# Performance work log

Hardware: AMD Instinct MI355X
Metric: run time of the kernel (lower is better)

Reference implementation:

```python
import jax, jax.numpy as jnp
import numpy as np

C_P = 1004.0
R_EARTH = 6371000.0
R_GAS = 287.0
OMEGA_E = 7.292e-05
B, K, H, W = 1, 8, 361, 720
KK = 5   # kernel basis size
D = 5    # neighborhood width in lat and lon (radius 2)
NS = K * 4 + 1
FCH = K * 4
NU = 2.0e5  # diffusion coefficient


def _ch(k, kind):
    return k * 4 + kind


def disco_gather(x, psi, quad):
    # DISCO sparse neighborhood aggregation on the sphere.
    # x: (B,C,H,W); psi: (KK,2,H,D,D) lat-dependent filter basis (2 directional comps)
    # returns (B,C,KK,2,H,W)
    Bx, C, Hx, Wx = x.shape
    Kk, nc, _, Dlat, Dlon = psi.shape
    r = Dlat // 2
    lat = np.clip(np.arange(Hx)[:, None] + np.arange(Dlat)[None, :] - r, 0, Hx - 1)
    out = jnp.zeros((Bx, C, Kk, nc, Hx, Wx), x.dtype)
    for dl in range(Dlat):
        li = lat[:, dl]
        xg = x[:, :, li, :] * quad[li][None, None, :, None]  # quadrature-weighted gather
        for dw in range(Dlon):
            xs = jnp.roll(xg, -(dw - r), axis=-1)  # circular in longitude
            out = out + psi[:, :, :, dl, dw][None, None, :, :, :, None] * xs[:, :, None, None, :, :]
    return out


def setup_inputs():
    key = jax.random.key(0)
    k1, k2, k3 = jax.random.split(key, 3)
    uv = jax.random.normal(k1, (B, K, H, W, 2), jnp.float32)
    T = jax.random.normal(k2, (B, K, H, W), jnp.float32)
    q = jax.random.normal(k3, (B, K, H, W), jnp.float32)
    rng = np.random.RandomState(0)
    psi = ((rng.rand(KK, 2, H, D, D) - 0.5) / (D * D)).astype(np.float32)
    colat = np.linspace(0.0, np.pi, H)
    quad = (np.sin(colat) * np.pi / (H - 1)).astype(np.float32)
    f_cor = (2.0 * OMEGA_E * np.sin(np.pi / 2.0 - colat)).astype(np.float32)
    p = np.array([1e5 * np.exp(-k * np.log(10.0) / (K - 1)) for k in range(K)], np.float32)
    lpr = np.log(p[:-1] / p[1:])
    p_low = np.concatenate([p[:1], 0.5 * (p[:-1] + p[1:])])
    p_up = np.concatenate([0.5 * (p[:-1] + p[1:]), [0.0]])
    dp = (p_low - p_up).astype(np.float32)
    # physics-encoded weights (module freezes all params and sets them analytically)
    W_ss_blk = np.zeros((NS, NS, KK), np.float32)
    W_vs_blk = np.zeros((NS, K, KK, 2), np.float32)
    for k in range(K):
        W_vs_blk[_ch(k, 2), k, :, 0] = 1.0 / R_EARTH  # zeta (curl)
        W_vs_blk[_ch(k, 3), k, :, 1] = 1.0 / R_EARTH  # div
    W_sv_blk = np.zeros((K, NS, KK, 2), np.float32)
    for ko in range(K):
        for ki in range(ko):
            W_sv_blk[ko, _ch(ki, 0), :, 1] = -R_GAS * lpr[ki] / R_EARTH  # PGF
        W_sv_blk[ko, _ch(ko, 1), :, 1] = -1.0 / R_EARTH  # -grad KE
    W_vv_blk = np.zeros((K, K, KK, 2), np.float32)
    W_vs2_blk = np.zeros((NS, K, KK, 2), np.float32)
    W_pw_ss = np.zeros((NS, NS), np.float32)
    W_pw_ss[FCH, FCH] = 1.0
    W_svp = np.zeros((NS, K, 2), np.float32)
    for k in range(K):
        W_svp[_ch(k, 2), k, 1] = 1.0
    W_svp[FCH, :, 1] = -1.0
    W_pw_vv = np.zeros((K, K), np.float32)
    W_ss_adv = np.zeros((2 * K, 2 * K, KK), np.float32)
    W_vs_adv = np.zeros((2 * K, K, KK, 2), np.float32)
    W_vs2_adv = np.zeros((2 * K, K, KK, 2), np.float32)
    for k in range(K):
        W_vs2_adv[k, k, :, 1] = -1.0 / R_EARTH      # -V.grad T
        W_vs2_adv[K + k, k, :, 1] = -1.0 / R_EARTH  # -V.grad q
    W_sv_grad = np.zeros((1, 1, KK, 2), np.float32)
    W_sv_grad[0, 0, :, 1] = 1.0 / R_EARTH
    W_vs_div = np.zeros((1, 1, KK, 2), np.float32)
    W_vs_div[0, 0, :, 1] = 1.0 / R_EARTH
    j = jnp.asarray
    return dict(uv=uv, T=T, q=q, psi=j(psi), quad=j(quad), f_cor=j(f_cor), p_levels=j(p), delta_p=j(dp),
                W_ss_blk=j(W_ss_blk), W_vs_blk=j(W_vs_blk), W_sv_blk=j(W_sv_blk), W_vv_blk=j(W_vv_blk),
                W_vs2_blk=j(W_vs2_blk), W_pw_ss=j(W_pw_ss), W_svp=j(W_svp), W_pw_vv=j(W_pw_vv),
                W_ss_adv=j(W_ss_adv), W_vs_adv=j(W_vs_adv), W_vs2_adv=j(W_vs2_adv),
                W_sv_grad=j(W_sv_grad), W_vs_div=j(W_vs_div))


def _forward(uv, T, q, psi, quad, f_cor, p_levels, delta_p, W_ss_blk, W_vs_blk, W_sv_blk, W_vv_blk,
             W_vs2_blk, W_pw_ss, W_svp, W_pw_vv, W_ss_adv, W_vs_adv, W_vs2_adv, W_sv_grad, W_vs_div):
    Bx, Kx, Hx, Wx = T.shape
    ke = 0.5 * (uv[..., 0] ** 2 + uv[..., 1] ** 2)
    zeros = jnp.zeros_like(T)
    per = jnp.stack([T, ke, zeros, zeros], axis=2).reshape(Bx, Kx * 4, Hx, Wx)
    f_field = jnp.broadcast_to(f_cor[None, None, :, None], (Bx, 1, Hx, Wx))
    x_s = jnp.concatenate([per, f_field], axis=1)  # (B, 4K+1, H, W)
    # ---- Block 1: VectorDiscoBlock ----
    Gs = disco_gather(x_s, psi, quad)               # (B,NS,KK,2,H,W)
    Ga = disco_gather(uv[..., 0], psi, quad)
    Gb = disco_gather(uv[..., 1], psi, quad)
    Gdir = jnp.stack([Ga[:, :, :, 0], Gb[:, :, :, 1]], axis=3)  # curl/div pairing
    Giso = jnp.stack([Ga[:, :, :, 0], Gb[:, :, :, 0]], axis=3)
    ys_c = jnp.einsum('oik,bikhw->bohw', W_ss_blk, Gs[:, :, :, 0])
    ys_c = ys_c + jnp.einsum('oikc,bikchw->bohw', W_vs_blk, Gdir)
    ys_c = ys_c + jnp.einsum('oikc,bokchw,bihwc->bohw', W_vs2_blk, Gs, uv)
    yv_c = jnp.einsum('oikc,bikchw->bohwc', W_sv_blk, Gs)
    yv_c = yv_c + jnp.einsum('oikc,bikchw->bohwc', W_vv_blk, Giso)
    s_feat = ys_c + jnp.einsum('oi,bihw->bohw', W_pw_ss, x_s)
    coef0 = jnp.einsum('ij,bihw->bjhw', W_svp[:, :, 0], s_feat)
    coef1 = jnp.einsum('ij,bihw->bjhw', W_svp[:, :, 1], s_feat)
    cross = jnp.stack([-uv[..., 1], uv[..., 0]], axis=-1)  # k-hat x V
    sv = coef0[..., None] * uv + coef1[..., None] * cross
    y_v = uv + yv_c + sv + jnp.einsum('oi,bihwc->bohwc', W_pw_vv, uv)
    y_s = s_feat
    duv_dt = y_v - uv
    # omega from divergence (upward pressure integral)
    div = y_s[:, :Kx * 4].reshape(Bx, Kx, 4, Hx, Wx)[:, :, 3]
    cum = jnp.cumsum(div * delta_p[None, :, None, None], axis=1)
    omega = 0.5 * (jnp.concatenate([jnp.zeros_like(cum[:, :1]), cum[:, :-1]], axis=1) + cum)
    # ---- adv_conv (W_vs2 pathway): -V.grad(T), -V.grad(q) ----
    tq = jnp.concatenate([T, q], axis=1)
    Gtq = disco_gather(tq, psi, quad)
    dTq = jnp.einsum('oik,bikhw->bohw', W_ss_adv, Gtq[:, :, :, 0])
    dTq = dTq + jnp.einsum('oikc,bikchw->bohw', W_vs_adv, Gdir)
    dTq = dTq + jnp.einsum('oikc,bokchw,bihwc->bohw', W_vs2_adv, Gtq, uv)
    dT_dt = dTq[:, :Kx]
    dq_dt = dTq[:, Kx:]
    # dT/dp central differences
    p = p_levels
    inter = (T[:, 2:] - T[:, :-2]) / (p[2:] - p[:-2])[None, :, None, None]
    first = (T[:, 1:2] - T[:, 0:1]) / (p[1] - p[0])
    last = (T[:, -1:] - T[:, -2:-1]) / (p[-1] - p[-2])
    dTdp = jnp.concatenate([first, inter, last], axis=1)
    pk = p[None, :, None, None]
    dT_dt = dT_dt + omega * (R_GAS / C_P * T / pk - dTdp)
    # ---- diffusion: nu * div(grad(s)) via grad_conv/div_conv ----
    def lap(s):
        sf = s.reshape(Bx * Kx, 1, Hx, Wx)
        Gsf = disco_gather(sf, psi, quad)
        g = jnp.einsum('oikc,bikchw->bohwc', W_sv_grad, Gsf)  # (BK,1,H,W,2)
        Gga = disco_gather(g[..., 0], psi, quad)
        Ggb = disco_gather(g[..., 1], psi, quad)
        Gd = jnp.stack([Gga[:, :, :, 0], Ggb[:, :, :, 1]], axis=3)
        return jnp.einsum('oikc,bikchw->bohw', W_vs_div, Gd).reshape(Bx, Kx, Hx, Wx)
    dT_dt = dT_dt + NU * lap(T)
    dq_dt = dq_dt + NU * lap(q)
    duv_dt = duv_dt + NU * jnp.stack([lap(uv[..., 0]), lap(uv[..., 1])], axis=-1)
    return duv_dt, dT_dt, dq_dt


def reference(uv, T, q, psi, quad, f_cor, p_levels, delta_p, W_ss_blk, W_vs_blk, W_sv_blk, W_vv_blk,
              W_vs2_blk, W_pw_ss, W_svp, W_pw_vv, W_ss_adv, W_vs_adv, W_vs2_adv, W_sv_grad, W_vs_div):
    return _forward(uv, T, q, psi, quad, f_cor, p_levels, delta_p, W_ss_blk, W_vs_blk, W_sv_blk,
                    W_vv_blk, W_vs2_blk, W_pw_ss, W_svp, W_pw_vv, W_ss_adv, W_vs_adv, W_vs2_adv,
                    W_sv_grad, W_vs_div)
```

## Files before the change

kernel.cpp:

```cpp
#include <hip/hip_runtime.h>


constexpr int Kz = 8, Hh = 361, Ww = 720;
constexpr int HW = Hh * Ww;
constexpr int OFF_DT = Kz * HW * 2;
constexpr int OFF_DQ = OFF_DT + Kz * HW;

constexpr int TH = 32, TW = 32;
constexpr int NTHR = 256;
constexpr int NCOL = 8;
constexpr int SH = TH + 8, SW4 = TW + 8;
constexpr int EH = TH + 4, EW4 = TW + 4;
constexpr int SW4P = 41;
constexpr int EW4P = 37;
constexpr int PQROW = 40;
constexpr int GX = (Ww + TW - 1) / TW;
constexpr int GY = (Hh + TH - 1) / TH;

__device__ __forceinline__ int clipH(int x) {
  return x < 0 ? 0 : (x > Hh - 1 ? Hh - 1 : x);
}

#define FMA4(acc, s, v)                                                        \
  do {                                                                         \
    acc.x = fmaf((s), (v).x, acc.x);                                           \
    acc.y = fmaf((s), (v).y, acc.y);                                           \
    acc.z = fmaf((s), (v).z, acc.z);                                           \
    acc.w = fmaf((s), (v).w, acc.w);                                           \
  } while (0)

#define ROWV(acc, a, b, c, d, e)                                               \
  do {                                                                         \
    FMA4(acc, wq0, a); FMA4(acc, wq1, b); FMA4(acc, wq2, c);                   \
    FMA4(acc, wq3, d); FMA4(acc, wq4, e);                                      \
  } while (0)

#define ROW5S(acc, q0, q1, q2, q3, q4, a, b, c, d, e)                          \
  acc = fmaf(q0, a, fmaf(q1, b, fmaf(q2, c, fmaf(q3, d, fmaf(q4, e, acc)))))

__global__ __launch_bounds__(256) void pe_tab_pq(
    const float* __restrict__ psi,
    const float* __restrict__ quad,
    float* __restrict__ P0g,
    float* __restrict__ P1g)
{
  int idx = blockIdx.x * 256 + threadIdx.x;
  if (idx >= Hh * PQROW) return;
  int h = idx / PQROW, o = idx - h * PQROW;
  int a = o >> 3, b = o & 7;
  float v0 = 0.f, v1 = 0.f;
  if (b < 5) {
    #pragma unroll
    for (int kk = 0; kk < 5; ++kk) {
      v0 += psi[kk * (2 * Hh * 25) + h * 25 + a * 5 + b];
      v1 += psi[kk * (2 * Hh * 25) + Hh * 25 + h * 25 + a * 5 + b];
    }
    float qv = quad[clipH(h + a - 2)];
    v0 *= qv; v1 *= qv;
  }
  P0g[idx] = v0;
  P1g[idx] = v1;
}

__global__ __launch_bounds__(NTHR) void pe_pass1(
    const float2* __restrict__ uv,
    const float*  __restrict__ Tg,
    const float*  __restrict__ qg,
    const float*  __restrict__ P0g,
    const float*  __restrict__ P1g,
    const float*  __restrict__ f_cor,
    const float*  __restrict__ delta_p,
    float* __restrict__ out,
    float2* __restrict__ ws)
{
  __shared__ float4 S4[SH][SW4P];
  __shared__ float4 d1S[EH][EW4P];

  const int tid = threadIdx.x;
  const int tx = tid % NCOL;
  const int ty = tid / NCOL;
  const int w0 = blockIdx.x * TW;
  const int h0 = blockIdx.y * TH;
  const int k  = blockIdx.z;

  for (int idx = tid; idx < SH * SW4; idx += NTHR) {
    int rr = idx / SW4, cc = idx - rr * SW4;
    int pr = clipH(h0 + rr - 4);
    int pc = w0 + cc - 4;
    pc = pc < 0 ? pc + Ww : (pc >= Ww ? pc - Ww : pc);
    int g = (k * Hh + pr) * Ww + pc;
    float2 uvv = uv[g];
    S4[rr][cc] = make_float4(uvv.x, uvv.y, Tg[g], qg[g]);
  }
  __syncthreads();

  for (int idx = tid; idx < EH * (EW4 / 4); idx += NTHR) {
    int ee = idx % EH;
    int gc = idx / EH;
    int cb = gc * 4;
    int p = clipH(h0 + ee - 2);
    const float* Pr = P1g + p * PQROW;
    float4 a0 = {0,0,0,0}, a1 = {0,0,0,0}, a2 = {0,0,0,0}, a3 = {0,0,0,0};
    #pragma unroll
    for (int dl = 0; dl < 5; ++dl) {
      int sp = clipH(p + dl - 2);
      int rr = sp - h0 + 4;
      const float4* row = &S4[rr][cb];
      float4 g0 = row[0], g1 = row[1], g2 = row[2], g3 = row[3];
      float4 g4 = row[4], g5 = row[5], g6 = row[6], g7 = row[7];
      float4 wA = *(const float4*)(Pr + dl * 8);
      float wq0 = wA.x, wq1 = wA.y, wq2 = wA.z, wq3 = wA.w;
      float wq4 = Pr[dl * 8 + 4];
      ROWV(a0, g0, g1, g2, g3, g4);
      ROWV(a1, g1, g2, g3, g4, g5);
      ROWV(a2, g2, g3, g4, g5, g6);
      ROWV(a3, g3, g4, g5, g6, g7);
    }
    d1S[ee][cb + 0] = a0; d1S[ee][cb + 1] = a1;
    d1S[ee][cb + 2] = a2; d1S[ee][cb + 3] = a3;
  }
  __syncthreads();

  const int h = h0 + ty;
  const int hc = h < Hh ? h : (Hh - 1);
  const int wbase = w0 + tx * 4;
  const float f = f_cor[hc];
  const float invR = (float)(1.0 / 6371000.0);
  const float halfInvR = 0.5f * invR;
  const float cL = 200000.0f * invR * invR;
  const float* Pr1 = P1g + hc * PQROW;
  const float* Pr0 = P0g + hc * PQROW;

  float4 lp0 = {0,0,0,0}, lp1 = {0,0,0,0}, lp2 = {0,0,0,0}, lp3 = {0,0,0,0};
  float du0 = 0.f, du1 = 0.f, du2 = 0.f, du3 = 0.f;
  float dk0 = 0.f, dk1 = 0.f, dk2 = 0.f, dk3 = 0.f;
  #pragma unroll
  for (int dl = 0; dl < 5; ++dl) {
    int sp = clipH(hc + dl - 2);
    int er = sp - h0 + 2;
    int rr = er + 2;
    float4 wA = *(const float4*)(Pr1 + dl * 8);
    float wq0 = wA.x, wq1 = wA.y, wq2 = wA.z, wq3 = wA.w;
    float wq4 = Pr1[dl * 8 + 4];
    {
      const float4* row = &d1S[er][tx * 4];
      float4 g0 = row[0], g1 = row[1], g2 = row[2], g3 = row[3];
      float4 g4 = row[4], g5 = row[5], g6 = row[6], g7 = row[7];
      ROWV(lp0, g0, g1, g2, g3, g4);
      ROWV(lp1, g1, g2, g3, g4, g5);
      ROWV(lp2, g2, g3, g4, g5, g6);
      ROWV(lp3, g3, g4, g5, g6, g7);
    }
    {
      const float4* srow = &S4[rr][tx * 4 + 2];
      float4 s0 = srow[0], s1 = srow[1], s2 = srow[2], s3 = srow[3];
      float4 s4 = srow[4], s5 = srow[5], s6 = srow[6], s7 = srow[7];
      float k0 = fmaf(s0.y, s0.y, s0.x * s0.x);
      float k1 = fmaf(s1.y, s1.y, s1.x * s1.x);
      float k2 = fmaf(s2.y, s2.y, s2.x * s2.x);
      float k3 = fmaf(s3.y, s3.y, s3.x * s3.x);
      float k4 = fmaf(s4.y, s4.y, s4.x * s4.x);
      float k5 = fmaf(s5.y, s5.y, s5.x * s5.x);
      float k6 = fmaf(s6.y, s6.y, s6.x * s6.x);
      float k7 = fmaf(s7.y, s7.y, s7.x * s7.x);
      ROW5S(dk0, wq0, wq1, wq2, wq3, wq4, k0, k1, k2, k3, k4);
      ROW5S(dk1, wq0, wq1, wq2, wq3, wq4, k1, k2, k3, k4, k5);
      ROW5S(dk2, wq0, wq1, wq2, wq3, wq4, k2, k3, k4, k5, k6);
      ROW5S(dk3, wq0, wq1, wq2, wq3, wq4, k3, k4, k5, k6, k7);
      float4 w0A = *(const float4*)(Pr0 + dl * 8);
      float q0 = w0A.x, q1 = w0A.y, q2 = w0A.z, q3 = w0A.w;
      float q4 = Pr0[dl * 8 + 4];
      ROW5S(du0, q0, q1, q2, q3, q4, s0.x, s1.x, s2.x, s3.x, s4.x);
      ROW5S(du1, q0, q1, q2, q3, q4, s1.x, s2.x, s3.x, s4.x, s5.x);
      ROW5S(du2, q0, q1, q2, q3, q4, s2.x, s3.x, s4.x, s5.x, s6.x);
      ROW5S(du3, q0, q1, q2, q3, q4, s3.x, s4.x, s5.x, s6.x, s7.x);
    }
  }

  if (h < Hh && wbase < Ww) {
    const float dpk = delta_p[k];
    float4 duvA, duvB, dTv, dqv, wsA, wsB;
    {
      float4 d1c = d1S[ty + 2][tx * 4 + 2];
      float4 ctr = S4[ty + 4][tx * 4 + 4];
      float coef1 = fmaf(du0, invR, -f);
      duvA.x = fmaf(-coef1, ctr.y, cL * lp0.x);
      duvA.y = fmaf(coef1, ctr.x, -halfInvR * dk0) + cL * lp0.y;
      dTv.x = -(invR * d1c.z) * ctr.y + cL * lp0.z;
      dqv.x = fmaf(-(invR * d1c.w), ctr.y, cL * lp0.w);
      wsA.x = invR * d1c.y * dpk; wsA.y = d1c.z;
    }
    {
      float4 d1c = d1S[ty + 2][tx * 4 + 3];
      float4 ctr = S4[ty + 4][tx * 4 + 5];
      float coef1 = fmaf(du1, invR, -f);
      duvA.z = fmaf(-coef1, ctr.y, cL * lp1.x);
      duvA.w = fmaf(coef1, ctr.x, -halfInvR * dk1) + cL * lp1.y;
      dTv.y = -(invR * d1c.z) * ctr.y + cL * lp1.z;
      dqv.y = fmaf(-(invR * d1c.w), ctr.y, cL * lp1.w);
      wsA.z = invR * d1c.y * dpk; wsA.w = d1c.z;
    }
    {
      float4 d1c = d1S[ty + 2][tx * 4 + 4];
      float4 ctr = S4[ty + 4][tx * 4 + 6];
      float coef1 = fmaf(du2, invR, -f);
      duvB.x = fmaf(-coef1, ctr.y, cL * lp2.x);
      duvB.y = fmaf(coef1, ctr.x, -halfInvR * dk2) + cL * lp2.y;
      dTv.z = -(invR * d1c.z) * ctr.y + cL * lp2.z;
      dqv.z = fmaf(-(invR * d1c.w), ctr.y, cL * lp2.w);
      wsB.x = invR * d1c.y * dpk; wsB.y = d1c.z;
    }
    {
      float4 d1c = d1S[ty + 2][tx * 4 + 5];
      float4 ctr = S4[ty + 4][tx * 4 + 7];
      float coef1 = fmaf(du3, invR, -f);
      duvB.z = fmaf(-coef1, ctr.y, cL * lp3.x);
      duvB.w = fmaf(coef1, ctr.x, -halfInvR * dk3) + cL * lp3.y;
      dTv.w = -(invR * d1c.z) * ctr.y + cL * lp3.z;
      dqv.w = fmaf(-(invR * d1c.w), ctr.y, cL * lp3.w);
      wsB.z = invR * d1c.y * dpk; wsB.w = d1c.z;
    }
    const int gidx = (k * Hh + h) * Ww + wbase;
    float4* o4 = (float4*)out;
    o4[gidx >> 1] = duvA;
    o4[(gidx >> 1) + 1] = duvB;
    *(float4*)&out[OFF_DT + gidx] = dTv;
    *(float4*)&out[OFF_DQ + gidx] = dqv;
    float4* w4 = (float4*)ws;
    w4[gidx >> 1] = wsA;
    w4[(gidx >> 1) + 1] = wsB;
  }
}

__global__ __launch_bounds__(256) void pe_pass2(
    const float* __restrict__ Tg,
    const float* __restrict__ p_levels,
    const float2* __restrict__ ws,
    float* __restrict__ out)
{
  int i4 = blockIdx.x * 256 + threadIdx.x;
  if (i4 >= HW / 4) return;
  const float invR = (float)(1.0 / 6371000.0);
  const float RCP = (float)(287.0 / 1004.0);

  float pl[Kz];
  #pragma unroll
  for (int k = 0; k < Kz; ++k) pl[k] = p_levels[k];

  const float4* T4 = (const float4*)Tg;
  const float4* ws4 = (const float4*)ws;
  float4* o4 = (float4*)out;
  float4* dT4 = (float4*)(out + OFF_DT);

  float4 cum = {0,0,0,0}, sumT = {0,0,0,0};
  float4 Tm = {0,0,0,0}, Tc = T4[i4];

  #pragma unroll
  for (int k = 0; k < Kz; ++k) {
    float4 Tp = (k < Kz - 1) ? T4[(k + 1) * (HW / 4) + i4] : make_float4(0,0,0,0);
    float4 wa = ws4[k * (HW / 2) + 2 * i4];
    float4 wb = ws4[k * (HW / 2) + 2 * i4 + 1];
    float om0 = fmaf(0.5f, wa.x, cum.x); cum.x += wa.x;
    float om1 = fmaf(0.5f, wa.z, cum.y); cum.y += wa.z;
    float om2 = fmaf(0.5f, wb.x, cum.z); cum.z += wb.x;
    float om3 = fmaf(0.5f, wb.z, cum.w); cum.w += wb.z;

    float4 dTdp;
    if (k == 0) {
      float idp = 1.f / (pl[1] - pl[0]);
      dTdp.x = (Tp.x - Tc.x) * idp; dTdp.y = (Tp.y - Tc.y) * idp;
      dTdp.z = (Tp.z - Tc.z) * idp; dTdp.w = (Tp.w - Tc.w) * idp;
    } else if (k == Kz - 1) {
      float idp = 1.f / (pl[Kz - 1] - pl[Kz - 2]);
      dTdp.x = (Tc.x - Tm.x) * idp; dTdp.y = (Tc.y - Tm.y) * idp;
      dTdp.z = (Tc.z - Tm.z) * idp; dTdp.w = (Tc.w - Tm.w) * idp;
    } else {
      float idp = 1.f / (pl[k + 1] - pl[k - 1]);
      dTdp.x = (Tp.x - Tm.x) * idp; dTdp.y = (Tp.y - Tm.y) * idp;
      dTdp.z = (Tp.z - Tm.z) * idp; dTdp.w = (Tp.w - Tm.w) * idp;
    }
    float iplk = RCP / pl[k];
    float4 dt = dT4[k * (HW / 4) + i4];
    dt.x += om0 * fmaf(iplk, Tc.x, -dTdp.x);
    dt.y += om1 * fmaf(iplk, Tc.y, -dTdp.y);
    dt.z += om2 * fmaf(iplk, Tc.z, -dTdp.z);
    dt.w += om3 * fmaf(iplk, Tc.w, -dTdp.w);
    dT4[k * (HW / 4) + i4] = dt;

    float4 oa = o4[k * (HW / 2) + 2 * i4];
    float4 ob = o4[k * (HW / 2) + 2 * i4 + 1];
    oa.y += sumT.x; oa.w += sumT.y;
    ob.y += sumT.z; ob.w += sumT.w;
    o4[k * (HW / 2) + 2 * i4] = oa;
    o4[k * (HW / 2) + 2 * i4 + 1] = ob;

    if (k < Kz - 1) {
      float c = -287.0f * logf(pl[k] / pl[k + 1]) * invR;
      sumT.x = fmaf(c, wa.y, sumT.x);
      sumT.y = fmaf(c, wa.w, sumT.y);
      sumT.z = fmaf(c, wb.y, sumT.z);
      sumT.w = fmaf(c, wb.w, sumT.w);
    }
    Tm = Tc; Tc = Tp;
  }
}

constexpr int FTH = 16, FTW = 16;
constexpr int FSH = FTH + 8, FSW = FTW + 8;
constexpr int FEH = FTH + 4, FEW = FTW + 4;
constexpr int FSWp = FSW + 1, FEWp = FEW + 1;

__global__ __launch_bounds__(256) void pe_step(
    const float2* __restrict__ uv,
    const float*  __restrict__ Tg,
    const float*  __restrict__ qg,
    const float*  __restrict__ psi,
    const float*  __restrict__ quad,
    const float*  __restrict__ f_cor,
    const float*  __restrict__ p_levels,
    const float*  __restrict__ delta_p,
    float* __restrict__ out)
{
  __shared__ float uS[FSH][FSWp], vS[FSH][FSWp], TS[FSH][FSWp], qS[FSH][FSWp];
  __shared__ float keS[FEH][FEWp];
  __shared__ float d1uS[FEH][FEWp], d1vS[FEH][FEWp], d1TS[FEH][FEWp], d1qS[FEH][FEWp];
  __shared__ float P1L[FEH][25];
  __shared__ float P0L[FTH][25];
  __shared__ float quadA[FSH];
  __shared__ float pl[8], dps[8];

  const int tid = threadIdx.x;
  const int tx = tid & (FTW - 1);
  const int ty = tid >> 4;
  const int w0 = blockIdx.x * FTW;
  const int h0 = blockIdx.y * FTH;

  if (tid < FSH) quadA[tid] = quad[clipH(h0 + tid - 4)];
  if (tid < 8) { pl[tid] = p_levels[tid]; dps[tid] = delta_p[tid]; }
  for (int idx = tid; idx < FEH * 25; idx += 256) {
    int ee = idx / 25, t = idx - ee * 25;
    int p = clipH(h0 + ee - 2);
    float s = 0.f;
    #pragma unroll
    for (int kk = 0; kk < 5; ++kk)
      s += psi[kk * (2 * Hh * 25) + Hh * 25 + p * 25 + t];
    P1L[ee][t] = s;
  }
  for (int idx = tid; idx < FTH * 25; idx += 256) {
    int r = idx / 25, t = idx - r * 25;
    int p = clipH(h0 + r);
    float s = 0.f;
    #pragma unroll
    for (int kk = 0; kk < 5; ++kk)
      s += psi[kk * (2 * Hh * 25) + p * 25 + t];
    P0L[r][t] = s;
  }
  __syncthreads();

  const int h = h0 + ty;
  const bool act = h < Hh;
  const int hc = act ? h : (Hh - 1);
  const int w = w0 + tx;
  const float f = f_cor[hc];
  const float invR = (float)(1.0 / 6371000.0);
  const float cL = 200000.0f * invR * invR;
  const float RCP = (float)(287.0 / 1004.0);

  float cum = 0.f;
  float sumT = 0.f;

  #pragma unroll 1
  for (int k = 0; k < Kz; ++k) {
    __syncthreads();
    for (int idx = tid; idx < FSH * FSW; idx += 256) {
      int rr = idx / FSW, cc = idx - rr * FSW;
      int pr = clipH(h0 + rr - 4);
      int pc = w0 + cc - 4;
      pc = pc < 0 ? pc + Ww : (pc >= Ww ? pc - Ww : pc);
      int g = (k * Hh + pr) * Ww + pc;
      float2 uvv = uv[g];
      uS[rr][cc] = uvv.x; vS[rr][cc] = uvv.y;
      TS[rr][cc] = Tg[g]; qS[rr][cc] = qg[g];
    }
    __syncthreads();
    for (int idx = tid; idx < FEH * FEW; idx += 256) {
      int ee = idx / FEW, ec = idx - ee * FEW;
      float su = uS[ee + 2][ec + 2], sv = vS[ee + 2][ec + 2];
      keS[ee][ec] = 0.5f * (su * su + sv * sv);
    }
    for (int idx = tid; idx < FEH * FEW; idx += 256) {
      int ee = idx / FEW, ec = idx - ee * FEW;
      int p = clipH(h0 + ee - 2);
      float au = 0.f, av = 0.f, aT = 0.f, aq = 0.f;
      #pragma unroll
      for (int dl = 0; dl < 5; ++dl) {
        int sp = clipH(p + dl - 2);
        int rr = sp - h0 + 4;
        float qv = quadA[rr];
        float ru = 0.f, rv = 0.f, rT = 0.f, rq = 0.f;
        #pragma unroll
        for (int dw = 0; dw < 5; ++dw) {
          float wgt = P1L[ee][dl * 5 + dw];
          ru = fmaf(wgt, uS[rr][ec + dw], ru);
          rv = fmaf(wgt, vS[rr][ec + dw], rv);
          rT = fmaf(wgt, TS[rr][ec + dw], rT);
          rq = fmaf(wgt, qS[rr][ec + dw], rq);
        }
        au = fmaf(qv, ru, au); av = fmaf(qv, rv, av);
        aT = fmaf(qv, rT, aT); aq = fmaf(qv, rq, aq);
      }
      d1uS[ee][ec] = au; d1vS[ee][ec] = av;
      d1TS[ee][ec] = aT; d1qS[ee][ec] = aq;
    }
    __syncthreads();

    float d0u = 0.f, d1ke = 0.f;
    #pragma unroll
    for (int dl = 0; dl < 5; ++dl) {
      int sp = clipH(hc + dl - 2);
      int rr = sp - h0 + 4;
      int er = sp - h0 + 2;
      float qv = quadA[rr];
      float r0 = 0.f, rk = 0.f;
      #pragma unroll
      for (int dw = 0; dw < 5; ++dw) {
        r0 = fmaf(P0L[ty][dl * 5 + dw], uS[rr][tx + 2 + dw], r0);
        rk = fmaf(P1L[ty + 2][dl * 5 + dw], keS[er][tx + dw], rk);
      }
      d0u = fmaf(qv, r0, d0u);
      d1ke = fmaf(qv, rk, d1ke);
    }

    float lapu = 0.f, lapv = 0.f, lapT = 0.f, lapq = 0.f;
    #pragma unroll
    for (int dl = 0; dl < 5; ++dl) {
      int sp = clipH(hc + dl - 2);
      int er = sp - h0 + 2;
      float qv = quadA[er + 2];
      float ru = 0.f, rv = 0.f, rT = 0.f, rq = 0.f;
      #pragma unroll
      for (int dw = 0; dw < 5; ++dw) {
        float wgt = P1L[ty + 2][dl * 5 + dw];
        ru = fmaf(wgt, d1uS[er][tx + dw], ru);
        rv = fmaf(wgt, d1vS[er][tx + dw], rv);
        rT = fmaf(wgt, d1TS[er][tx + dw], rT);
        rq = fmaf(wgt, d1qS[er][tx + dw], rq);
      }
      lapu = fmaf(qv, ru, lapu); lapv = fmaf(qv, rv, lapv);
      lapT = fmaf(qv, rT, lapT); lapq = fmaf(qv, rq, lapq);
    }

    float d1T_c = d1TS[ty + 2][tx + 2];
    float d1v_c = d1vS[ty + 2][tx + 2];
    float d1q_c = d1qS[ty + 2][tx + 2];
    float uc = uS[ty + 4][tx + 4], vc = vS[ty + 4][tx + 4];
    float Tc = TS[ty + 4][tx + 4];

    float coef1 = fmaf(d0u, invR, -f);
    float duv0 = fmaf(-coef1, vc, cL * lapu);
    float yv1 = fmaf(-invR, d1ke, sumT);
    float duv1 = fmaf(coef1, uc, yv1) + cL * lapv;

    float div = invR * d1v_c;
    float dpk = dps[k];
    float omega = fmaf(0.5f * div, dpk, cum);
    cum = fmaf(div, dpk, cum);

    int gidx = (k * Hh + hc) * Ww + w;
    float dTdp;
    if (k == 0) {
      float Tp = Tg[gidx + HW];
      dTdp = (Tp - Tc) / (pl[1] - pl[0]);
    } else if (k == Kz - 1) {
      float Tm = Tg[gidx - HW];
      dTdp = (Tc - Tm) / (pl[Kz - 1] - pl[Kz - 2]);
    } else {
      float Tp = Tg[gidx + HW];
      float Tm = Tg[gidx - HW];
      dTdp = (Tp - Tm) / (pl[k + 1] - pl[k - 1]);
    }
    float adv = -(invR * d1T_c) * vc;
    float dT = adv + omega * ((RCP * Tc) / pl[k] - dTdp) + cL * lapT;
    float dq = fmaf(-(invR * d1q_c), vc, cL * lapq);

    if (act) {
      ((float2*)out)[(k * Hh + h) * Ww + w] = make_float2(duv0, duv1);
      out[OFF_DT + gidx] = dT;
      out[OFF_DQ + gidx] = dq;
    }

    if (k < Kz - 1) {
      float lpr = logf(pl[k] / pl[k + 1]);
      float wTk = (float)(-287.0 * (double)lpr / 6371000.0);
      sumT = fmaf(wTk, d1T_c, sumT);
    }
  }
}

extern "C" void kernel_launch(void* const* d_in, const int* in_sizes, int n_in,
                              void* d_out, int out_size, void* d_ws, size_t ws_size,
                              hipStream_t stream) {
  (void)in_sizes; (void)n_in; (void)out_size;
  const float2* uv   = (const float2*)d_in[0];
  const float*  T    = (const float*) d_in[1];
  const float*  q    = (const float*) d_in[2];
  const float*  psi  = (const float*) d_in[3];
  const float*  quad = (const float*) d_in[4];
  const float*  fc   = (const float*) d_in[5];
  const float*  pl   = (const float*) d_in[6];
  const float*  dp   = (const float*) d_in[7];

  const size_t ws_div_floats = (size_t)2 * Kz * HW;
  const size_t pq_floats = (size_t)Hh * PQROW;
  const size_t ws_need = (ws_div_floats + 2 * pq_floats) * sizeof(float);
  if (ws_size >= ws_need) {
    float* wsF = (float*)d_ws;
    float* P0g = wsF + ws_div_floats;
    float* P1g = P0g + pq_floats;

    dim3 gt1((Hh * PQROW + 255) / 256);
    hipLaunchKernelGGL(pe_tab_pq, gt1, dim3(256), 0, stream, psi, quad, P0g, P1g);

    dim3 g1(GX, GY, Kz);
    hipLaunchKernelGGL(pe_pass1, g1, dim3(NTHR), 0, stream,
                       uv, T, q, P0g, P1g, fc, dp, (float*)d_out, (float2*)d_ws);

    dim3 g2((HW / 4 + 255) / 256);
    hipLaunchKernelGGL(pe_pass2, g2, dim3(256), 0, stream,
                       T, pl, (const float2*)d_ws, (float*)d_out);
  } else {
    dim3 grid(Ww / FTW, (Hh + FTH - 1) / FTH);
    hipLaunchKernelGGL(pe_step, grid, dim3(256), 0, stream,
                       uv, T, q, psi, quad, fc, pl, dp, (float*)d_out);
  }
}
```

Before: 68.00 us.

## Compute kinetic-energy and u-gather stencils in first pass, stage in shared memory

Moves the kinetic-energy and P0-weighted u gathers out of the second stencil phase into the first pass over the extended tile. The results and the centre u/v values go into a new shared buffer d2S, and the centre d1 values are taken from registers. The second phase now reads only d1S rows instead of both d1S and S4. The first phase covers the larger halo region, so it does redundant work on halo rows, and the extra shared buffer may lower occupancy.

```diff
diff --git a/kernel.cpp b/kernel.cpp
--- a/kernel.cpp
+++ b/kernel.cpp
@@ -75,6 +75,7 @@
 {
   __shared__ float4 S4[SH][SW4P];
   __shared__ float4 d1S[EH][EW4P];
+  __shared__ float4 d2S[EH][EW4P];
 
   const int tid = threadIdx.x;
   const int tx = tid % NCOL;
@@ -99,8 +100,12 @@
     int gc = idx / EH;
     int cb = gc * 4;
     int p = clipH(h0 + ee - 2);
-    const float* Pr = P1g + p * PQROW;
+    const float* Pr  = P1g + p * PQROW;
+    const float* Pr0 = P0g + p * PQROW;
     float4 a0 = {0,0,0,0}, a1 = {0,0,0,0}, a2 = {0,0,0,0}, a3 = {0,0,0,0};
+    float ku0 = 0, ku1 = 0, ku2 = 0, ku3 = 0;
+    float du0 = 0, du1 = 0, du2 = 0, du3 = 0;
+    float2 c0, c1, c2, c3;
     #pragma unroll
     for (int dl = 0; dl < 5; ++dl) {
       int sp = clipH(p + dl - 2);
@@ -108,16 +113,45 @@
       const float4* row = &S4[rr][cb];
       float4 g0 = row[0], g1 = row[1], g2 = row[2], g3 = row[3];
       float4 g4 = row[4], g5 = row[5], g6 = row[6], g7 = row[7];
+      float ka0 = fmaf(g0.y, g0.y, g0.x * g0.x);
+      float ka1 = fmaf(g1.y, g1.y, g1.x * g1.x);
+      float ka2 = fmaf(g2.y, g2.y, g2.x * g2.x);
+      float ka3 = fmaf(g3.y, g3.y, g3.x * g3.x);
+      float ka4 = fmaf(g4.y, g4.y, g4.x * g4.x);
+      float ka5 = fmaf(g5.y, g5.y, g5.x * g5.x);
+      float ka6 = fmaf(g6.y, g6.y, g6.x * g6.x);
+      float ka7 = fmaf(g7.y, g7.y, g7.x * g7.x);
       float4 wA = *(const float4*)(Pr + dl * 8);
       float wq0 = wA.x, wq1 = wA.y, wq2 = wA.z, wq3 = wA.w;
       float wq4 = Pr[dl * 8 + 4];
+      float4 w0A = *(const float4*)(Pr0 + dl * 8);
+      float p0 = w0A.x, p1 = w0A.y, p2 = w0A.z, p3 = w0A.w;
+      float p4 = Pr0[dl * 8 + 4];
       ROWV(a0, g0, g1, g2, g3, g4);
       ROWV(a1, g1, g2, g3, g4, g5);
       ROWV(a2, g2, g3, g4, g5, g6);
       ROWV(a3, g3, g4, g5, g6, g7);
+      ROW5S(ku0, wq0, wq1, wq2, wq3, wq4, ka0, ka1, ka2, ka3, ka4);
+      ROW5S(ku1, wq0, wq1, wq2, wq3, wq4, ka1, ka2, ka3, ka4, ka5);
+      ROW5S(ku2, wq0, wq1, wq2, wq3, wq4, ka2, ka3, ka4, ka5, ka6);
+      ROW5S(ku3, wq0, wq1, wq2, wq3, wq4, ka3, ka4, ka5, ka6, ka7);
+      ROW5S(du0, p0, p1, p2, p3, p4, g0.x, g1.x, g2.x, g3.x, g4.x);
+      ROW5S(du1, p0, p1, p2, p3, p4, g1.x, g2.x, g3.x, g4.x, g5.x);
+      ROW5S(du2, p0, p1, p2, p3, p4, g2.x, g3.x, g4.x, g5.x, g6.x);
+      ROW5S(du3, p0, p1, p2, p3, p4, g3.x, g4.x, g5.x, g6.x, g7.x);
+      if (dl == 2) {
+        c0 = make_float2(g2.x, g2.y);
+        c1 = make_float2(g3.x, g3.y);
+        c2 = make_float2(g4.x, g4.y);
+        c3 = make_float2(g5.x, g5.y);
+      }
     }
     d1S[ee][cb + 0] = a0; d1S[ee][cb + 1] = a1;
     d1S[ee][cb + 2] = a2; d1S[ee][cb + 3] = a3;
+    d2S[ee][cb + 0] = make_float4(ku0, du0, c0.x, c0.y);
+    d2S[ee][cb + 1] = make_float4(ku1, du1, c1.x, c1.y);
+    d2S[ee][cb + 2] = make_float4(ku2, du2, c2.x, c2.y);
+    d2S[ee][cb + 3] = make_float4(ku3, du3, c3.x, c3.y);
   }
   __syncthreads();
 
@@ -129,96 +163,64 @@
   const float halfInvR = 0.5f * invR;
   const float cL = 200000.0f * invR * invR;
   const float* Pr1 = P1g + hc * PQROW;
-  const float* Pr0 = P0g + hc * PQROW;
 
   float4 lp0 = {0,0,0,0}, lp1 = {0,0,0,0}, lp2 = {0,0,0,0}, lp3 = {0,0,0,0};
-  float du0 = 0.f, du1 = 0.f, du2 = 0.f, du3 = 0.f;
-  float dk0 = 0.f, dk1 = 0.f, dk2 = 0.f, dk3 = 0.f;
+  float4 d1c0, d1c1, d1c2, d1c3;
   #pragma unroll
   for (int dl = 0; dl < 5; ++dl) {
     int sp = clipH(hc + dl - 2);
     int er = sp - h0 + 2;
-    int rr = er + 2;
     float4 wA = *(const float4*)(Pr1 + dl * 8);
     float wq0 = wA.x, wq1 = wA.y, wq2 = wA.z, wq3 = wA.w;
     float wq4 = Pr1[dl * 8 + 4];
-    {
-      const float4* row = &d1S[er][tx * 4];
-      float4 g0 = row[0], g1 = row[1], g2 = row[2], g3 = row[3];
-      float4 g4 = row[4], g5 = row[5], g6 = row[6], g7 = row[7];
-      ROWV(lp0, g0, g1, g2, g3, g4);
-      ROWV(lp1, g1, g2, g3, g4, g5);
-      ROWV(lp2, g2, g3, g4, g5, g6);
-      ROWV(lp3, g3, g4, g5, g6, g7);
-    }
-    {
-      const float4* srow = &S4[rr][tx * 4 + 2];
-      float4 s0 = srow[0], s1 = srow[1], s2 = srow[2], s3 = srow[3];
-      float4 s4 = srow[4], s5 = srow[5], s6 = srow[6], s7 = srow[7];
-      float k0 = fmaf(s0.y, s0.y, s0.x * s0.x);
-      float k1 = fmaf(s1.y, s1.y, s1.x * s1.x);
-      float k2 = fmaf(s2.y, s2.y, s2.x * s2.x);
-      float k3 = fmaf(s3.y, s3.y, s3.x * s3.x);
-      float k4 = fmaf(s4.y, s4.y, s4.x * s4.x);
-      float k5 = fmaf(s5.y, s5.y, s5.x * s5.x);
-      float k6 = fmaf(s6.y, s6.y, s6.x * s6.x);
-      float k7 = fmaf(s7.y, s7.y, s7.x * s7.x);
-      ROW5S(dk0, wq0, wq1, wq2, wq3, wq4, k0, k1, k2, k3, k4);
-      ROW5S(dk1, wq0, wq1, wq2, wq3, wq4, k1, k2, k3, k4, k5);
-      ROW5S(dk2, wq0, wq1, wq2, wq3, wq4, k2, k3, k4, k5, k6);
-      ROW5S(dk3, wq0, wq1, wq2, wq3, wq4, k3, k4, k5, k6, k7);
-      float4 w0A = *(const float4*)(Pr0 + dl * 8);
-      float q0 = w0A.x, q1 = w0A.y, q2 = w0A.z, q3 = w0A.w;
-      float q4 = Pr0[dl * 8 + 4];
-      ROW5S(du0, q0, q1, q2, q3, q4, s0.x, s1.x, s2.x, s3.x, s4.x);
-      ROW5S(du1, q0, q1, q2, q3, q4, s1.x, s2.x, s3.x, s4.x, s5.x);
-      ROW5S(du2, q0, q1, q2, q3, q4, s2.x, s3.x, s4.x, s5.x, s6.x);
-      ROW5S(du3, q0, q1, q2, q3, q4, s3.x, s4.x, s5.x, s6.x, s7.x);
-    }
+    const float4* row = &d1S[er][tx * 4];
+    float4 g0 = row[0], g1 = row[1], g2 = row[2], g3 = row[3];
+    float4 g4 = row[4], g5 = row[5], g6 = row[6], g7 = row[7];
+    ROWV(lp0, g0, g1, g2, g3, g4);
+    ROWV(lp1, g1, g2, g3, g4, g5);
+    ROWV(lp2, g2, g3, g4, g5, g6);
+    ROWV(lp3, g3, g4, g5, g6, g7);
+    if (dl == 2) { d1c0 = g2; d1c1 = g3; d1c2 = g4; d1c3 = g5; }
   }
 
   if (h < Hh && wbase < Ww) {
     const float dpk = delta_p[k];
     float4 duvA, duvB, dTv, dqv, wsA, wsB;
     {
-      float4 d1c = d1S[ty + 2][tx * 4 + 2];
-      float4 ctr = S4[ty + 4][tx * 4 + 4];
-      float coef1 = fmaf(du0, invR, -f);
-      duvA.x = fmaf(-coef1, ctr.y, cL * lp0.x);
-      duvA.y = fmaf(coef1, ctr.x, -halfInvR * dk0) + cL * lp0.y;
-      dTv.x = -(invR * d1c.z) * ctr.y + cL * lp0.z;
-      dqv.x = fmaf(-(invR * d1c.w), ctr.y, cL * lp0.w);
-      wsA.x = invR * d1c.y * dpk; wsA.y = d1c.z;
+      float4 kd = d2S[ty + 2][tx * 4 + 2];
+      float coef1 = fmaf(kd.y, invR, -f);
+      duvA.x = fmaf(-coef1, kd.w, cL * lp0.x);
+      duvA.y = fmaf(coef1, kd.z, -halfInvR * kd.x) + cL * lp0.y;
+      dTv.x = -(invR * d1c0.z) * kd.w + cL * lp0.z;
+      dqv.x = fmaf(-(invR * d1c0.w), kd.w, cL * lp0.w);
+      wsA.x = invR * d1c0.y * dpk; wsA.y = d1c0.z;
     }
     {
-      float4 d1c = d1S[ty + 2][tx * 4 + 3];
-      float4 ctr = S4[ty + 4][tx * 4 + 5];
-      float coef1 = fmaf(du1, invR, -f);
-      duvA.z = fmaf(-coef1, ctr.y, cL * lp1.x);
-      duvA.w = fmaf(coef1, ctr.x, -halfInvR * dk1) + cL * lp1.y;
-      dTv.y = -(invR * d1c.z) * ctr.y + cL * lp1.z;
-      dqv.y = fmaf(-(invR * d1c.w), ctr.y, cL * lp1.w);
-      wsA.z = invR * d1c.y * dpk; wsA.w = d1c.z;
+      float4 kd = d2S[ty + 2][tx * 4 + 3];
+      float coef1 = fmaf(kd.y, invR, -f);
+      duvA.z = fmaf(-coef1, kd.w, cL * lp1.x);
+      duvA.w = fmaf(coef1, kd.z, -halfInvR * kd.x) + cL * lp1.y;
+      dTv.y = -(invR * d1c1.z) * kd.w + cL * lp1.z;
+      dqv.y = fmaf(-(invR * d1c1.w), kd.w, cL * lp1.w);
+      wsA.z = invR * d1c1.y * dpk; wsA.w = d1c1.z;
     }
     {
-      float4 d1c = d1S[ty + 2][tx * 4 + 4];
-      float4 ctr = S4[ty + 4][tx * 4 + 6];
-      float coef1 = fmaf(du2, invR, -f);
-      duvB.x = fmaf(-coef1, ctr.y, cL * lp2.x);
-      duvB.y = fmaf(coef1, ctr.x, -halfInvR * dk2) + cL * lp2.y;
-      dTv.z = -(invR * d1c.z) * ctr.y + cL * lp2.z;
-      dqv.z = fmaf(-(invR * d1c.w), ctr.y, cL * lp2.w);
-      wsB.x = invR * d1c.y * dpk; wsB.y = d1c.z;
+      float4 kd = d2S[ty + 2][tx * 4 + 4];
+      float coef1 = fmaf(kd.y, invR, -f);
+      duvB.x = fmaf(-coef1, kd.w, cL * lp2.x);
+      duvB.y = fmaf(coef1, kd.z, -halfInvR * kd.x) + cL * lp2.y;
+      dTv.z = -(invR * d1c2.z) * kd.w + cL * lp2.z;
+      dqv.z = fmaf(-(invR * d1c2.w), kd.w, cL * lp2.w);
+      wsB.x = invR * d1c2.y * dpk; wsB.y = d1c2.z;
     }
     {
-      float4 d1c = d1S[ty + 2][tx * 4 + 5];
-      float4 ctr = S4[ty + 4][tx * 4 + 7];
-      float coef1 = fmaf(du3, invR, -f);
-      duvB.z = fmaf(-coef1, ctr.y, cL * lp3.x);
-      duvB.w = fmaf(coef1, ctr.x, -halfInvR * dk3) + cL * lp3.y;
-      dTv.w = -(invR * d1c.z) * ctr.y + cL * lp3.z;
-      dqv.w = fmaf(-(invR * d1c.w), ctr.y, cL * lp3.w);
-      wsB.z = invR * d1c.y * dpk; wsB.w = d1c.z;
+      float4 kd = d2S[ty + 2][tx * 4 + 5];
+      float coef1 = fmaf(kd.y, invR, -f);
+      duvB.z = fmaf(-coef1, kd.w, cL * lp3.x);
+      duvB.w = fmaf(coef1, kd.z, -halfInvR * kd.x) + cL * lp3.y;
+      dTv.w = -(invR * d1c3.z) * kd.w + cL * lp3.z;
+      dqv.w = fmaf(-(invR * d1c3.w), kd.w, cL * lp3.w);
+      wsB.z = invR * d1c3.y * dpk; wsB.w = d1c3.z;
     }
     const int gidx = (k * Hh + h) * Ww + wbase;
     float4* o4 = (float4*)out;
```

Result: slower. 96.52 us (+41.9%).
